# Kernel optimization log

Measured on AMD Instinct MI355X. Metric: run time of the kernel, lower is better.

The kernel has to match this reference:

```python
import jax, jax.numpy as jnp
import numpy as np


def setup_inputs() -> dict:
    key = jax.random.key(0)
    ks = jax.random.split(key, 8)
    B, S, Nc, C, Cseed = 4, 4096, 8192, 512, 256
    return {
        "query_xyz": jax.random.normal(ks[0], (B, S, 3), dtype=jnp.float32),
        "ref_xyz": jax.random.normal(ks[1], (B, Nc, 3), dtype=jnp.float32),
        "ref_feat": jax.random.normal(ks[2], (B, C, Nc), dtype=jnp.float32),
        "seed_features": jax.random.normal(ks[3], (B, Cseed, S), dtype=jnp.float32),
        "W_seed_proj": jax.random.normal(ks[4], (Cseed, C), dtype=jnp.float32) * 0.02,
        "b_seed_proj": jax.random.normal(ks[5], (Cseed,), dtype=jnp.float32) * 0.02,
        "W_concat_proj": jax.random.normal(ks[6], (Cseed, 2 * Cseed), dtype=jnp.float32) * 0.02,
        "b_concat_proj": jax.random.normal(ks[7], (Cseed,), dtype=jnp.float32) * 0.02,
    }


def _nn_gather(query_xyz, ref_xyz, ref_feat):
    # torch.cdist(p=2) + argmin: argmin over squared distance is identical
    # (sqrt is monotonic), so we skip the sqrt.
    q2 = jnp.sum(query_xyz * query_xyz, axis=-1, keepdims=True)      # (B,S,1)
    r2 = jnp.sum(ref_xyz * ref_xyz, axis=-1)[:, None, :]             # (B,1,Nc)
    qr = jnp.einsum("bsd,bnd->bsn", query_xyz, ref_xyz)              # (B,S,Nc)
    d2 = q2 + r2 - 2.0 * qr                                          # (B,S,Nc)
    idx = jnp.argmin(d2, axis=-1)                                    # (B,S) int
    # gather nearest-neighbor features: (B,C,Nc) -> (B,C,S)
    return jnp.take_along_axis(ref_feat, idx[:, None, :], axis=2)


def reference(query_xyz, ref_xyz, ref_feat, seed_features,
              W_seed_proj, b_seed_proj, W_concat_proj, b_concat_proj):
    lift3d_raw = _nn_gather(query_xyz, ref_xyz, ref_feat)            # (B,C,S)
    # 1x1 Conv1d == channel matmul
    lift3d_seed = jnp.einsum("oc,bcs->bos", W_seed_proj, lift3d_raw) \
                  + b_seed_proj[None, :, None]                       # (B,256,S)
    fused = jnp.concatenate([seed_features, lift3d_seed], axis=1)    # (B,512,S)
    out = jnp.einsum("oc,bcs->bos", W_concat_proj, fused) \
          + b_concat_proj[None, :, None]                             # (B,256,S)
    return out
```

## Files before the change

### kernel.cpp

```cpp
#include <hip/hip_runtime.h>

#define B_   4
#define S_   4096
#define NC   8192
#define C_   512
#define CS   256
#define KTOT 768

typedef __attribute__((ext_vector_type(8))) short short8;
typedef __attribute__((ext_vector_type(4))) float f32x4;

static __device__ __forceinline__ unsigned short f2bf(float x) {
    unsigned u = __builtin_bit_cast(unsigned, x);
    unsigned r = u + 0x7FFFu + ((u >> 16) & 1u);
    return (unsigned short)(r >> 16);
}

__global__ __launch_bounds__(256) void prep_kernel(
        const float* __restrict__ rxyz, float4* __restrict__ refpk,
        const float* __restrict__ Wcat, const float* __restrict__ Wseed,
        unsigned short* __restrict__ Wcomb,
        const float* __restrict__ bseed, const float* __restrict__ bcat,
        float* __restrict__ beff) {
    __shared__ float sa[64][68];
    __shared__ float sbt[64][68];
    int bid = blockIdx.x;
    int tid = threadIdx.x;

    if (bid < 64) {
        int w = tid >> 6, l = tid & 63;
        int o = bid * 4 + w;
        float4 wv = *(const float4*)(Wcat + (size_t)o * 512 + 256 + l * 4);
        float4 bb = *(const float4*)(bseed + l * 4);
        float acc = __fmul_rn(wv.x, bb.x);
        acc = fmaf(wv.y, bb.y, acc);
        acc = fmaf(wv.z, bb.z, acc);
        acc = fmaf(wv.w, bb.w, acc);
        #pragma unroll
        for (int off = 32; off > 0; off >>= 1) acc += __shfl_down(acc, off);
        if (l == 0) beff[o] = acc + bcat[o];
    } else if (bid < 96) {
        int xb = bid - 64;
        int tc = (xb & 7) * 64;
        int to = (xb >> 3) * 64;
        int tx = tid & 15, ty = tid >> 4;
        float acc[4][4] = {};
        for (int kt = 0; kt < 256; kt += 64) {
            __syncthreads();
            #pragma unroll
            for (int r = 0; r < 4; ++r) {
                int oo = r * 16 + ty;
                float4 v = *(const float4*)(Wcat + (size_t)(to + oo) * 512 + 256 + kt + tx * 4);
                sa[oo][tx * 4 + 0] = v.x;
                sa[oo][tx * 4 + 1] = v.y;
                sa[oo][tx * 4 + 2] = v.z;
                sa[oo][tx * 4 + 3] = v.w;
                float4 u = *(const float4*)(Wseed + (size_t)(kt + oo) * 512 + tc + tx * 4);
                sbt[oo][tx * 4 + 0] = u.x;
                sbt[oo][tx * 4 + 1] = u.y;
                sbt[oo][tx * 4 + 2] = u.z;
                sbt[oo][tx * 4 + 3] = u.w;
            }
            __syncthreads();
            for (int k = 0; k < 64; ++k) {
                float a[4], bb2[4];
                #pragma unroll
                for (int i = 0; i < 4; ++i) a[i] = sa[ty * 4 + i][k];
                #pragma unroll
                for (int j = 0; j < 4; ++j) bb2[j] = sbt[k][tx * 4 + j];
                #pragma unroll
                for (int i = 0; i < 4; ++i)
                    #pragma unroll
                    for (int j = 0; j < 4; ++j)
                        acc[i][j] = fmaf(a[i], bb2[j], acc[i][j]);
            }
        }
        #pragma unroll
        for (int i = 0; i < 4; ++i)
            #pragma unroll
            for (int j = 0; j < 4; ++j)
                Wcomb[(size_t)(to + ty * 4 + i) * KTOT + 256 + tc + tx * 4 + j] = f2bf(acc[i][j]);
    } else if (bid < 160) {
        int g = ((bid - 96) * 256 + tid) * 4;
        int o = g >> 8, cc = g & 255;
        float4 v = *(const float4*)(Wcat + (size_t)o * 512 + cc);
        ushort4 ov;
        ov.x = f2bf(v.x); ov.y = f2bf(v.y); ov.z = f2bf(v.z); ov.w = f2bf(v.w);
        *(ushort4*)(Wcomb + (size_t)o * KTOT + cc) = ov;
    } else {
        int gid = (bid - 160) * 256 + tid;
        float x = rxyz[gid * 3 + 0];
        float y = rxyz[gid * 3 + 1];
        float z = rxyz[gid * 3 + 2];
        float r2 = __fadd_rn(__fadd_rn(__fmul_rn(x, x), __fmul_rn(y, y)), __fmul_rn(z, z));
        refpk[gid] = make_float4(x, y, z, r2);
    }
}

__global__ __launch_bounds__(256, 4) void mid_kernel(
        const float* __restrict__ qxyz, const float4* __restrict__ refpk,
        float* __restrict__ pval, int* __restrict__ pidx,
        const float* __restrict__ rf, unsigned short* __restrict__ refT) {
    __shared__ float t[64][65];
    int bid = blockIdx.x;
    int tid = threadIdx.x;

    if (bid % 3 != 0) {
        int id = bid - bid / 3 - 1;
        int b = id >> 10;
        int c0 = ((id >> 7) & 7) * 64;
        int n0 = (id & 127) * 64;
        int tx = tid & 15, ty = tid >> 4;
        #pragma unroll
        for (int r = 0; r < 4; ++r) {
            int cc = r * 16 + ty;
            float4 v = *(const float4*)(rf + ((size_t)b * C_ + c0 + cc) * NC + n0 + tx * 4);
            t[tx * 4 + 0][cc] = v.x;
            t[tx * 4 + 1][cc] = v.y;
            t[tx * 4 + 2][cc] = v.z;
            t[tx * 4 + 3][cc] = v.w;
        }
        __syncthreads();
        #pragma unroll
        for (int r = 0; r < 4; ++r) {
            int n = r * 16 + ty;
            ushort4 o;
            o.x = f2bf(t[n][tx * 4 + 0]);
            o.y = f2bf(t[n][tx * 4 + 1]);
            o.z = f2bf(t[n][tx * 4 + 2]);
            o.w = f2bf(t[n][tx * 4 + 3]);
            *(ushort4*)(refT + ((size_t)b * NC + n0 + n) * C_ + c0 + tx * 4) = o;
        }
    } else {
        int aid = bid / 3;
        int sblk = aid & 127;
        int c = (aid >> 7) & 3;
        int b = aid >> 9;
        int lane = tid & 63;
        int qg = tid >> 6;
        int sbase = sblk * 32 + qg * 8;

        float qx[8], qy[8], qz[8], q2[8];
        #pragma unroll
        for (int q = 0; q < 8; ++q) {
            const float* qp = qxyz + ((size_t)(b * S_ + sbase + q)) * 3;
            qx[q] = qp[0]; qy[q] = qp[1]; qz[q] = qp[2];
            q2[q] = __fadd_rn(__fadd_rn(__fmul_rn(qx[q], qx[q]), __fmul_rn(qy[q], qy[q])),
                              __fmul_rn(qz[q], qz[q]));
        }

        const float4* ep = refpk + (size_t)b * NC + c * 2048 + lane;
        float best[8];
        int bj[8];
        #pragma unroll
        for (int q = 0; q < 8; ++q) { best[q] = 3.4028235e38f; bj[q] = 0; }

        float4 r0 = ep[0];
        float4 r1 = ep[64];
        #pragma unroll 2
        for (int j = 0; j < 32; j += 2) {
            float4 r2 = r0, r3 = r1;
            if (j + 2 < 32) {
                r2 = ep[(j + 2) * 64];
                r3 = ep[(j + 3) * 64];
            }
            #pragma unroll
            for (int q = 0; q < 8; ++q) {
                float qr = __fadd_rn(__fadd_rn(__fmul_rn(qx[q], r0.x), __fmul_rn(qy[q], r0.y)),
                                     __fmul_rn(qz[q], r0.z));
                float s = __fadd_rn(q2[q], r0.w);
                float d2 = fmaf(qr, -2.0f, s);
                if (d2 < best[q]) { best[q] = d2; bj[q] = j; }
            }
            #pragma unroll
            for (int q = 0; q < 8; ++q) {
                float qr = __fadd_rn(__fadd_rn(__fmul_rn(qx[q], r1.x), __fmul_rn(qy[q], r1.y)),
                                     __fmul_rn(qz[q], r1.z));
                float s = __fadd_rn(q2[q], r1.w);
                float d2 = fmaf(qr, -2.0f, s);
                if (d2 < best[q]) { best[q] = d2; bj[q] = j + 1; }
            }
            r0 = r2;
            r1 = r3;
        }

        int bx[8];
        #pragma unroll
        for (int q = 0; q < 8; ++q) bx[q] = c * 2048 + bj[q] * 64 + lane;

        #pragma unroll
        for (int m = 1; m < 64; m <<= 1) {
            #pragma unroll
            for (int q = 0; q < 8; ++q) {
                float vv = __shfl_xor(best[q], m, 64);
                int xx = __shfl_xor(bx[q], m, 64);
                if (vv < best[q] || (vv == best[q] && xx < bx[q])) {
                    best[q] = vv; bx[q] = xx;
                }
            }
        }
        if (lane == 0) {
            #pragma unroll
            for (int q = 0; q < 8; ++q) {
                int qs = b * S_ + sbase + q;
                pval[qs * 4 + c] = best[q];
                pidx[qs * 4 + c] = bx[q];
            }
        }
    }
}

__global__ __launch_bounds__(256) void fused_gemm_kernel(
        const unsigned short* __restrict__ Wcomb,
        const float* __restrict__ seed,
        const unsigned short* __restrict__ refT,
        const float* __restrict__ pval,
        const int* __restrict__ pidx,
        const float* __restrict__ beff,
        float* __restrict__ out) {
    __shared__ __align__(16) unsigned short sA[2][128][72];
    __shared__ __align__(16) unsigned short sB[2][32][72];
    __shared__ int sIdx[32];
    __shared__ float sBias[128];

    int tid = threadIdx.x;
    int b = blockIdx.z;
    int m0 = blockIdx.y * 128;
    int s0 = blockIdx.x * 32;
    if (tid < 32) {
        int qs = b * S_ + s0 + tid;
        float v = pval[qs * 4 + 0];
        int x = pidx[qs * 4 + 0];
        #pragma unroll
        for (int c = 1; c < 4; ++c) {
            float vv = pval[qs * 4 + c];
            int xx = pidx[qs * 4 + c];
            if (vv < v || (vv == v && xx < x)) { v = vv; x = xx; }
        }
        sIdx[tid] = x & (NC - 1);
    }
    if (tid < 128) sBias[tid] = beff[m0 + tid];

    int lane = tid & 63;
    int w = tid >> 6;
    int ln = lane & 15;
    int quad = lane >> 4;
    int q8 = quad * 8;

    int mmb  = tid >> 3;
    int kk8a = (tid & 7) << 3;
    const unsigned short* Arow = Wcomb + (size_t)(m0 + mmb) * KTOT + kk8a;
    int n_s  = tid & 31;
    int kk8s = (tid >> 5) << 3;
    int n_g  = tid >> 3;

    f32x4 acc[2][2];
    #pragma unroll
    for (int i = 0; i < 2; ++i)
        #pragma unroll
        for (int j = 0; j < 2; ++j)
            acc[i][j] = (f32x4){0.f, 0.f, 0.f, 0.f};

    short8 ra[4];
    short8 rb;
    float rbf[8];

    #define SLOAD(PK) do {                                                         \
        int pk0 = (PK) * 64;                                                       \
        _Pragma("unroll")                                                          \
        for (int i = 0; i < 4; ++i)                                                \
            ra[i] = *(const short8*)(Arow + (size_t)i * 32 * KTOT + pk0);          \
        if (pk0 < 256) {                                                           \
            const float* sp = seed + ((size_t)b * CS + pk0 + kk8s) * S_ + s0 + n_s;\
            _Pragma("unroll")                                                      \
            for (int r = 0; r < 8; ++r) rbf[r] = sp[(size_t)r * S_];               \
        } else {                                                                   \
            rb = *(const short8*)(refT + ((size_t)b * NC + sIdx[n_g]) * C_         \
                                  + (pk0 - 256) + kk8a);                           \
        }                                                                          \
    } while (0)

    #define SWRITE(BUF, PK) do {                                                   \
        int pk0 = (PK) * 64;                                                       \
        _Pragma("unroll")                                                          \
        for (int i = 0; i < 4; ++i)                                                \
            *(short8*)&sA[BUF][mmb + 32 * i][kk8a] = ra[i];                        \
        if (pk0 < 256) {                                                           \
            unsigned short tmp[8];                                                 \
            _Pragma("unroll")                                                      \
            for (int r = 0; r < 8; ++r) tmp[r] = f2bf(rbf[r]);                     \
            *(short8*)&sB[BUF][n_s][kk8s] = *(const short8*)tmp;                   \
        } else {                                                                   \
            *(short8*)&sB[BUF][n_g][kk8a] = rb;                                    \
        }                                                                          \
    } while (0)

    SLOAD(0);
    SWRITE(0, 0);
    __syncthreads();

    int cur = 0;
    for (int ks = 0; ks < 12; ++ks) {
        if (ks < 11) SLOAD(ks + 1);
        #pragma unroll
        for (int kf = 0; kf < 2; ++kf) {
            short8 af[2], bfr[2];
            #pragma unroll
            for (int i = 0; i < 2; ++i)
                af[i] = *(const short8*)&sA[cur][w * 32 + i * 16 + ln][kf * 32 + q8];
            #pragma unroll
            for (int j = 0; j < 2; ++j)
                bfr[j] = *(const short8*)&sB[cur][j * 16 + ln][kf * 32 + q8];
            #pragma unroll
            for (int i = 0; i < 2; ++i)
                #pragma unroll
                for (int j = 0; j < 2; ++j)
                    acc[i][j] = __builtin_amdgcn_mfma_f32_16x16x32_bf16(af[i], bfr[j], acc[i][j], 0, 0, 0);
        }
        if (ks < 11) {
            SWRITE(cur ^ 1, ks + 1);
            __syncthreads();
            cur ^= 1;
        }
    }
    #undef SLOAD
    #undef SWRITE

    #pragma unroll
    for (int i = 0; i < 2; ++i) {
        int mb = w * 32 + i * 16 + quad * 4;
        #pragma unroll
        for (int j = 0; j < 2; ++j) {
            int col = s0 + j * 16 + ln;
            #pragma unroll
            for (int r = 0; r < 4; ++r) {
                int m = mb + r;
                out[((size_t)b * CS + m0 + m) * S_ + col] = acc[i][j][r] + sBias[m];
            }
        }
    }
}

extern "C" void kernel_launch(void* const* d_in, const int* in_sizes, int n_in,
                              void* d_out, int out_size, void* d_ws, size_t ws_size,
                              hipStream_t stream) {
    const float* qxyz  = (const float*)d_in[0];
    const float* rxyz  = (const float*)d_in[1];
    const float* rfeat = (const float*)d_in[2];
    const float* seed  = (const float*)d_in[3];
    const float* Wseed = (const float*)d_in[4];
    const float* bseed = (const float*)d_in[5];
    const float* Wcat  = (const float*)d_in[6];
    const float* bcat  = (const float*)d_in[7];
    float* out = (float*)d_out;

    char* ws = (char*)d_ws;
    float* pval           = (float*)(ws);
    int* pidx             = (int*)(ws + 262144);
    float* beff           = (float*)(ws + 524288);
    float4* refpk         = (float4*)(ws + 528384);
    unsigned short* Wcomb = (unsigned short*)(ws + 1052672);
    unsigned short* refT  = (unsigned short*)(ws + 1445888);

    hipLaunchKernelGGL(prep_kernel, dim3(288), dim3(256), 0, stream,
                       rxyz, refpk, Wcat, Wseed, Wcomb, bseed, bcat, beff);
    hipLaunchKernelGGL(mid_kernel, dim3(6144), dim3(256), 0, stream,
                       qxyz, refpk, pval, pidx, rfeat, refT);
    hipLaunchKernelGGL(fused_gemm_kernel, dim3(128, 2, 4), dim3(256), 0, stream,
                       Wcomb, seed, refT, pval, pidx, beff, out);
}
```

Before: 189.2 us.

## Move seed-feature GEMM half into mid kernel, overlapping with NN search

The seed_features half of the concat projection (K=256) moves out of the final GEMM. A new prep stage transposes seed into bf16 seedT, and mid_kernel gains a third block type that computes the Wcomb[:, :256] x seedT partial product and writes it to out, running alongside the NN search and refT transpose blocks. The final GEMM then only covers the gathered refT half (8 k-steps instead of 12) and adds the partial result read back from out. This trades an extra read and write of out, plus a seed transpose pass, for a shorter critical-path GEMM and for overlapping independent work. It also drops the occupancy hint on mid_kernel.

```diff
diff --git a/kernel.cpp b/kernel.cpp
--- a/kernel.cpp
+++ b/kernel.cpp
@@ -21,7 +21,8 @@
         const float* __restrict__ Wcat, const float* __restrict__ Wseed,
         unsigned short* __restrict__ Wcomb,
         const float* __restrict__ bseed, const float* __restrict__ bcat,
-        float* __restrict__ beff) {
+        float* __restrict__ beff,
+        const float* __restrict__ seed, unsigned short* __restrict__ seedT) {
     __shared__ float sa[64][68];
     __shared__ float sbt[64][68];
     int bid = blockIdx.x;
@@ -87,26 +88,179 @@
         ushort4 ov;
         ov.x = f2bf(v.x); ov.y = f2bf(v.y); ov.z = f2bf(v.z); ov.w = f2bf(v.w);
         *(ushort4*)(Wcomb + (size_t)o * KTOT + cc) = ov;
-    } else {
+    } else if (bid < 288) {
         int gid = (bid - 160) * 256 + tid;
         float x = rxyz[gid * 3 + 0];
         float y = rxyz[gid * 3 + 1];
         float z = rxyz[gid * 3 + 2];
         float r2 = __fadd_rn(__fadd_rn(__fmul_rn(x, x), __fmul_rn(y, y)), __fmul_rn(z, z));
         refpk[gid] = make_float4(x, y, z, r2);
+    } else {
+        int id = bid - 288;
+        int b = id >> 8;
+        int rem = id & 255;
+        int c0 = (rem >> 6) * 64;
+        int s0 = (rem & 63) * 64;
+        int tx = tid & 15, ty = tid >> 4;
+        #pragma unroll
+        for (int r = 0; r < 4; ++r) {
+            int cc = r * 16 + ty;
+            float4 v = *(const float4*)(seed + ((size_t)b * CS + c0 + cc) * S_ + s0 + tx * 4);
+            sa[tx * 4 + 0][cc] = v.x;
+            sa[tx * 4 + 1][cc] = v.y;
+            sa[tx * 4 + 2][cc] = v.z;
+            sa[tx * 4 + 3][cc] = v.w;
+        }
+        __syncthreads();
+        #pragma unroll
+        for (int r = 0; r < 4; ++r) {
+            int n = r * 16 + ty;
+            ushort4 o;
+            o.x = f2bf(sa[n][tx * 4 + 0]);
+            o.y = f2bf(sa[n][tx * 4 + 1]);
+            o.z = f2bf(sa[n][tx * 4 + 2]);
+            o.w = f2bf(sa[n][tx * 4 + 3]);
+            *(ushort4*)(seedT + ((size_t)b * S_ + s0 + n) * CS + c0 + tx * 4) = o;
+        }
     }
 }
 
-__global__ __launch_bounds__(256, 4) void mid_kernel(
+__global__ __launch_bounds__(256) void mid_kernel(
         const float* __restrict__ qxyz, const float4* __restrict__ refpk,
         float* __restrict__ pval, int* __restrict__ pidx,
-        const float* __restrict__ rf, unsigned short* __restrict__ refT) {
-    __shared__ float t[64][65];
+        const float* __restrict__ rf, unsigned short* __restrict__ refT,
+        const unsigned short* __restrict__ Wcomb,
+        const unsigned short* __restrict__ seedT,
+        float* __restrict__ out) {
+    __shared__ __align__(16) char smem[16640];
     int bid = blockIdx.x;
     int tid = threadIdx.x;
-
-    if (bid % 3 != 0) {
-        int id = bid - bid / 3 - 1;
+    int r4 = bid & 3;
+    int g = bid >> 2;
+
+    if (r4 == 0) {
+        int aid = g;
+        int sblk = aid & 127;
+        int c = (aid >> 7) & 3;
+        int b = aid >> 9;
+        int lane = tid & 63;
+        int qg = tid >> 6;
+        int sbase = sblk * 32 + qg * 8;
+
+        float qx[8], qy[8], qz[8], q2[8];
+        #pragma unroll
+        for (int q = 0; q < 8; ++q) {
+            const float* qp = qxyz + ((size_t)(b * S_ + sbase + q)) * 3;
+            qx[q] = qp[0]; qy[q] = qp[1]; qz[q] = qp[2];
+            q2[q] = __fadd_rn(__fadd_rn(__fmul_rn(qx[q], qx[q]), __fmul_rn(qy[q], qy[q])),
+                              __fmul_rn(qz[q], qz[q]));
+        }
+
+        const float4* ep = refpk + (size_t)b * NC + c * 2048 + lane;
+        float best[8];
+        int bj[8];
+        #pragma unroll
+        for (int q = 0; q < 8; ++q) { best[q] = 3.4028235e38f; bj[q] = 0; }
+
+        float4 r0 = ep[0];
+        float4 r1 = ep[64];
+        #pragma unroll 2
+        for (int j = 0; j < 32; j += 2) {
+            float4 r2 = r0, r3 = r1;
+            if (j + 2 < 32) {
+                r2 = ep[(j + 2) * 64];
+                r3 = ep[(j + 3) * 64];
+            }
+            #pragma unroll
+            for (int q = 0; q < 8; ++q) {
+                float qr = __fadd_rn(__fadd_rn(__fmul_rn(qx[q], r0.x), __fmul_rn(qy[q], r0.y)),
+                                     __fmul_rn(qz[q], r0.z));
+                float s = __fadd_rn(q2[q], r0.w);
+                float d2 = fmaf(qr, -2.0f, s);
+                if (d2 < best[q]) { best[q] = d2; bj[q] = j; }
+            }
+            #pragma unroll
+            for (int q = 0; q < 8; ++q) {
+                float qr = __fadd_rn(__fadd_rn(__fmul_rn(qx[q], r1.x), __fmul_rn(qy[q], r1.y)),
+                                     __fmul_rn(qz[q], r1.z));
+                float s = __fadd_rn(q2[q], r1.w);
+                float d2 = fmaf(qr, -2.0f, s);
+                if (d2 < best[q]) { best[q] = d2; bj[q] = j + 1; }
+            }
+            r0 = r2;
+            r1 = r3;
+        }
+
+        int bx[8];
+        #pragma unroll
+        for (int q = 0; q < 8; ++q) bx[q] = c * 2048 + bj[q] * 64 + lane;
+
+        #pragma unroll
+        for (int m = 1; m < 64; m <<= 1) {
+            #pragma unroll
+            for (int q = 0; q < 8; ++q) {
+                float vv = __shfl_xor(best[q], m, 64);
+                int xx = __shfl_xor(bx[q], m, 64);
+                if (vv < best[q] || (vv == best[q] && xx < bx[q])) {
+                    best[q] = vv; bx[q] = xx;
+                }
+            }
+        }
+        if (lane == 0) {
+            #pragma unroll
+            for (int q = 0; q < 8; ++q) {
+                int qs = b * S_ + sbase + q;
+                pval[qs * 4 + c] = best[q];
+                pidx[qs * 4 + c] = bx[q];
+            }
+        }
+    } else if (r4 == 2) {
+        unsigned short (*sAw)[72] = (unsigned short (*)[72])smem;
+        unsigned short (*sBw)[72] = (unsigned short (*)[72])(smem + 9216);
+        int b = g >> 9;
+        int rem = g & 511;
+        int m0 = (rem >> 7) * 64;
+        int s0 = (rem & 127) * 32;
+        int lane = tid & 63;
+        int w = tid >> 6;
+        int ln = lane & 15;
+        int quad = lane >> 4;
+        int q8 = quad * 8;
+        int mm = tid >> 2, kk16 = (tid & 3) << 4;
+        int n = tid >> 3, kk8 = (tid & 7) << 3;
+        const unsigned short* Ar = Wcomb + (size_t)(m0 + mm) * KTOT + kk16;
+        const unsigned short* Br = seedT + ((size_t)b * S_ + s0 + n) * CS + kk8;
+
+        f32x4 acc2[2];
+        acc2[0] = (f32x4){0.f, 0.f, 0.f, 0.f};
+        acc2[1] = (f32x4){0.f, 0.f, 0.f, 0.f};
+        for (int kt = 0; kt < 4; ++kt) {
+            __syncthreads();
+            *(short8*)&sAw[mm][kk16]     = *(const short8*)(Ar + kt * 64);
+            *(short8*)&sAw[mm][kk16 + 8] = *(const short8*)(Ar + kt * 64 + 8);
+            *(short8*)&sBw[n][kk8]       = *(const short8*)(Br + kt * 64);
+            __syncthreads();
+            #pragma unroll
+            for (int kf = 0; kf < 2; ++kf) {
+                short8 af = *(const short8*)&sAw[w * 16 + ln][kf * 32 + q8];
+                #pragma unroll
+                for (int j = 0; j < 2; ++j) {
+                    short8 bfr = *(const short8*)&sBw[j * 16 + ln][kf * 32 + q8];
+                    acc2[j] = __builtin_amdgcn_mfma_f32_16x16x32_bf16(af, bfr, acc2[j], 0, 0, 0);
+                }
+            }
+        }
+        int mb = m0 + w * 16 + quad * 4;
+        #pragma unroll
+        for (int j = 0; j < 2; ++j) {
+            int col = s0 + j * 16 + ln;
+            #pragma unroll
+            for (int r = 0; r < 4; ++r)
+                out[((size_t)b * CS + mb + r) * S_ + col] = acc2[j][r];
+        }
+    } else {
+        float (*t)[65] = (float (*)[65])smem;
+        int id = g * 2 + (r4 >> 1);
         int b = id >> 10;
         int c0 = ((id >> 7) & 7) * 64;
         int n0 = (id & 127) * 64;
@@ -131,88 +285,11 @@
             o.w = f2bf(t[n][tx * 4 + 3]);
             *(ushort4*)(refT + ((size_t)b * NC + n0 + n) * C_ + c0 + tx * 4) = o;
         }
-    } else {
-        int aid = bid / 3;
-        int sblk = aid & 127;
-        int c = (aid >> 7) & 3;
-        int b = aid >> 9;
-        int lane = tid & 63;
-        int qg = tid >> 6;
-        int sbase = sblk * 32 + qg * 8;
-
-        float qx[8], qy[8], qz[8], q2[8];
-        #pragma unroll
-        for (int q = 0; q < 8; ++q) {
-            const float* qp = qxyz + ((size_t)(b * S_ + sbase + q)) * 3;
-            qx[q] = qp[0]; qy[q] = qp[1]; qz[q] = qp[2];
-            q2[q] = __fadd_rn(__fadd_rn(__fmul_rn(qx[q], qx[q]), __fmul_rn(qy[q], qy[q])),
-                              __fmul_rn(qz[q], qz[q]));
-        }
-
-        const float4* ep = refpk + (size_t)b * NC + c * 2048 + lane;
-        float best[8];
-        int bj[8];
-        #pragma unroll
-        for (int q = 0; q < 8; ++q) { best[q] = 3.4028235e38f; bj[q] = 0; }
-
-        float4 r0 = ep[0];
-        float4 r1 = ep[64];
-        #pragma unroll 2
-        for (int j = 0; j < 32; j += 2) {
-            float4 r2 = r0, r3 = r1;
-            if (j + 2 < 32) {
-                r2 = ep[(j + 2) * 64];
-                r3 = ep[(j + 3) * 64];
-            }
-            #pragma unroll
-            for (int q = 0; q < 8; ++q) {
-                float qr = __fadd_rn(__fadd_rn(__fmul_rn(qx[q], r0.x), __fmul_rn(qy[q], r0.y)),
-                                     __fmul_rn(qz[q], r0.z));
-                float s = __fadd_rn(q2[q], r0.w);
-                float d2 = fmaf(qr, -2.0f, s);
-                if (d2 < best[q]) { best[q] = d2; bj[q] = j; }
-            }
-            #pragma unroll
-            for (int q = 0; q < 8; ++q) {
-                float qr = __fadd_rn(__fadd_rn(__fmul_rn(qx[q], r1.x), __fmul_rn(qy[q], r1.y)),
-                                     __fmul_rn(qz[q], r1.z));
-                float s = __fadd_rn(q2[q], r1.w);
-                float d2 = fmaf(qr, -2.0f, s);
-                if (d2 < best[q]) { best[q] = d2; bj[q] = j + 1; }
-            }
-            r0 = r2;
-            r1 = r3;
-        }
-
-        int bx[8];
-        #pragma unroll
-        for (int q = 0; q < 8; ++q) bx[q] = c * 2048 + bj[q] * 64 + lane;
-
-        #pragma unroll
-        for (int m = 1; m < 64; m <<= 1) {
-            #pragma unroll
-            for (int q = 0; q < 8; ++q) {
-                float vv = __shfl_xor(best[q], m, 64);
-                int xx = __shfl_xor(bx[q], m, 64);
-                if (vv < best[q] || (vv == best[q] && xx < bx[q])) {
-                    best[q] = vv; bx[q] = xx;
-                }
-            }
-        }
-        if (lane == 0) {
-            #pragma unroll
-            for (int q = 0; q < 8; ++q) {
-                int qs = b * S_ + sbase + q;
-                pval[qs * 4 + c] = best[q];
-                pidx[qs * 4 + c] = bx[q];
-            }
-        }
     }
 }
 
 __global__ __launch_bounds__(256) void fused_gemm_kernel(
         const unsigned short* __restrict__ Wcomb,
-        const float* __restrict__ seed,
         const unsigned short* __restrict__ refT,
         const float* __restrict__ pval,
         const int* __restrict__ pidx,
@@ -249,9 +326,7 @@
 
     int mmb  = tid >> 3;
     int kk8a = (tid & 7) << 3;
-    const unsigned short* Arow = Wcomb + (size_t)(m0 + mmb) * KTOT + kk8a;
-    int n_s  = tid & 31;
-    int kk8s = (tid >> 5) << 3;
+    const unsigned short* Arow = Wcomb + (size_t)(m0 + mmb) * KTOT + 256 + kk8a;
     int n_g  = tid >> 3;
 
     f32x4 acc[2][2];
@@ -263,45 +338,31 @@
 
     short8 ra[4];
     short8 rb;
-    float rbf[8];
 
     #define SLOAD(PK) do {                                                         \
         int pk0 = (PK) * 64;                                                       \
         _Pragma("unroll")                                                          \
         for (int i = 0; i < 4; ++i)                                                \
             ra[i] = *(const short8*)(Arow + (size_t)i * 32 * KTOT + pk0);          \
-        if (pk0 < 256) {                                                           \
-            const float* sp = seed + ((size_t)b * CS + pk0 + kk8s) * S_ + s0 + n_s;\
-            _Pragma("unroll")                                                      \
-            for (int r = 0; r < 8; ++r) rbf[r] = sp[(size_t)r * S_];               \
-        } else {                                                                   \
-            rb = *(const short8*)(refT + ((size_t)b * NC + sIdx[n_g]) * C_         \
-                                  + (pk0 - 256) + kk8a);                           \
-        }                                                                          \
+        rb = *(const short8*)(refT + ((size_t)b * NC + sIdx[n_g]) * C_             \
+                              + pk0 + kk8a);                                       \
     } while (0)
 
-    #define SWRITE(BUF, PK) do {                                                   \
-        int pk0 = (PK) * 64;                                                       \
+    #define SWRITE(BUF) do {                                                       \
         _Pragma("unroll")                                                          \
         for (int i = 0; i < 4; ++i)                                                \
             *(short8*)&sA[BUF][mmb + 32 * i][kk8a] = ra[i];                        \
-        if (pk0 < 256) {                                                           \
-            unsigned short tmp[8];                                                 \
-            _Pragma("unroll")                                                      \
-            for (int r = 0; r < 8; ++r) tmp[r] = f2bf(rbf[r]);                     \
-            *(short8*)&sB[BUF][n_s][kk8s] = *(const short8*)tmp;                   \
-        } else {                                                                   \
-            *(short8*)&sB[BUF][n_g][kk8a] = rb;                                    \
-        }                                                                          \
+        *(short8*)&sB[BUF][n_g][kk8a] = rb;                                        \
     } while (0)
 
+    __syncthreads();
     SLOAD(0);
-    SWRITE(0, 0);
+    SWRITE(0);
     __syncthreads();
 
     int cur = 0;
-    for (int ks = 0; ks < 12; ++ks) {
-        if (ks < 11) SLOAD(ks + 1);
+    for (int ks = 0; ks < 8; ++ks) {
+        if (ks < 7) SLOAD(ks + 1);
         #pragma unroll
         for (int kf = 0; kf < 2; ++kf) {
             short8 af[2], bfr[2];
@@ -317,8 +378,8 @@
                 for (int j = 0; j < 2; ++j)
                     acc[i][j] = __builtin_amdgcn_mfma_f32_16x16x32_bf16(af[i], bfr[j], acc[i][j], 0, 0, 0);
         }
-        if (ks < 11) {
-            SWRITE(cur ^ 1, ks + 1);
+        if (ks < 7) {
+            SWRITE(cur ^ 1);
             __syncthreads();
             cur ^= 1;
         }
@@ -335,7 +396,8 @@
             #pragma unroll
             for (int r = 0; r < 4; ++r) {
                 int m = mb + r;
-                out[((size_t)b * CS + m0 + m) * S_ + col] = acc[i][j][r] + sBias[m];
+                size_t oaddr = ((size_t)b * CS + m0 + m) * S_ + col;
+                out[oaddr] = acc[i][j][r] + sBias[m] + out[oaddr];
             }
         }
     }
@@ -361,11 +423,12 @@
     float4* refpk         = (float4*)(ws + 528384);
     unsigned short* Wcomb = (unsigned short*)(ws + 1052672);
     unsigned short* refT  = (unsigned short*)(ws + 1445888);
-
-    hipLaunchKernelGGL(prep_kernel, dim3(288), dim3(256), 0, stream,
-                       rxyz, refpk, Wcat, Wseed, Wcomb, bseed, bcat, beff);
-    hipLaunchKernelGGL(mid_kernel, dim3(6144), dim3(256), 0, stream,
-                       qxyz, refpk, pval, pidx, rfeat, refT);
+    unsigned short* seedT = (unsigned short*)(ws + 35000320);
+
+    hipLaunchKernelGGL(prep_kernel, dim3(1312), dim3(256), 0, stream,
+                       rxyz, refpk, Wcat, Wseed, Wcomb, bseed, bcat, beff, seed, seedT);
+    hipLaunchKernelGGL(mid_kernel, dim3(8192), dim3(256), 0, stream,
+                       qxyz, refpk, pval, pidx, rfeat, refT, Wcomb, seedT, out);
     hipLaunchKernelGGL(fused_gemm_kernel, dim3(128, 2, 4), dim3(256), 0, stream,
-                       Wcomb, seed, refT, pval, pidx, beff, out);
+                       Wcomb, refT, pval, pidx, beff, out);
 }
```

New measurement: 251.9 us. 1.33x slower.

## Pre-transpose seed features to bf16 and retile fused GEMM to 64x64 single-buffered

Applied to the files above, without the earlier changes.

Adds blocks to the prep kernel that transpose seed_features into an S-major bf16 buffer. The fused GEMM can then load both B sources with contiguous 16-byte vector loads instead of strided fp32 reads converted in-kernel. The GEMM tile changes from 128x32 to 64x64 with a 2x2 wave layout, and the double-buffered register prefetch is removed in favour of a simple sync-load-sync loop. The cost is an extra transpose pass over seed data and less overlap between global loads and MFMA work.

```diff
diff --git a/kernel.cpp b/kernel.cpp
--- a/kernel.cpp
+++ b/kernel.cpp
@@ -21,7 +21,8 @@
         const float* __restrict__ Wcat, const float* __restrict__ Wseed,
         unsigned short* __restrict__ Wcomb,
         const float* __restrict__ bseed, const float* __restrict__ bcat,
-        float* __restrict__ beff) {
+        float* __restrict__ beff,
+        const float* __restrict__ seed, unsigned short* __restrict__ seedT) {
     __shared__ float sa[64][68];
     __shared__ float sbt[64][68];
     int bid = blockIdx.x;
@@ -87,13 +88,40 @@
         ushort4 ov;
         ov.x = f2bf(v.x); ov.y = f2bf(v.y); ov.z = f2bf(v.z); ov.w = f2bf(v.w);
         *(ushort4*)(Wcomb + (size_t)o * KTOT + cc) = ov;
-    } else {
+    } else if (bid < 288) {
         int gid = (bid - 160) * 256 + tid;
         float x = rxyz[gid * 3 + 0];
         float y = rxyz[gid * 3 + 1];
         float z = rxyz[gid * 3 + 2];
         float r2 = __fadd_rn(__fadd_rn(__fmul_rn(x, x), __fmul_rn(y, y)), __fmul_rn(z, z));
         refpk[gid] = make_float4(x, y, z, r2);
+    } else {
+        int id = bid - 288;
+        int b = id >> 8;
+        int rem = id & 255;
+        int c0 = (rem >> 6) * 64;
+        int s0 = (rem & 63) * 64;
+        int tx = tid & 15, ty = tid >> 4;
+        #pragma unroll
+        for (int r = 0; r < 4; ++r) {
+            int cc = r * 16 + ty;
+            float4 v = *(const float4*)(seed + ((size_t)b * CS + c0 + cc) * S_ + s0 + tx * 4);
+            sa[tx * 4 + 0][cc] = v.x;
+            sa[tx * 4 + 1][cc] = v.y;
+            sa[tx * 4 + 2][cc] = v.z;
+            sa[tx * 4 + 3][cc] = v.w;
+        }
+        __syncthreads();
+        #pragma unroll
+        for (int r = 0; r < 4; ++r) {
+            int n = r * 16 + ty;
+            ushort4 o;
+            o.x = f2bf(sa[n][tx * 4 + 0]);
+            o.y = f2bf(sa[n][tx * 4 + 1]);
+            o.z = f2bf(sa[n][tx * 4 + 2]);
+            o.w = f2bf(sa[n][tx * 4 + 3]);
+            *(ushort4*)(seedT + ((size_t)b * S_ + s0 + n) * CS + c0 + tx * 4) = o;
+        }
     }
 }
 
@@ -212,22 +240,22 @@
 
 __global__ __launch_bounds__(256) void fused_gemm_kernel(
         const unsigned short* __restrict__ Wcomb,
-        const float* __restrict__ seed,
+        const unsigned short* __restrict__ seedT,
         const unsigned short* __restrict__ refT,
         const float* __restrict__ pval,
         const int* __restrict__ pidx,
         const float* __restrict__ beff,
         float* __restrict__ out) {
-    __shared__ __align__(16) unsigned short sA[2][128][72];
-    __shared__ __align__(16) unsigned short sB[2][32][72];
-    __shared__ int sIdx[32];
-    __shared__ float sBias[128];
+    __shared__ __align__(16) unsigned short sA[64][72];
+    __shared__ __align__(16) unsigned short sB[64][72];
+    __shared__ int sIdx[64];
+    __shared__ float sBias[64];
 
     int tid = threadIdx.x;
     int b = blockIdx.z;
-    int m0 = blockIdx.y * 128;
-    int s0 = blockIdx.x * 32;
-    if (tid < 32) {
+    int m0 = blockIdx.y * 64;
+    int s0 = blockIdx.x * 64;
+    if (tid < 64) {
         int qs = b * S_ + s0 + tid;
         float v = pval[qs * 4 + 0];
         int x = pidx[qs * 4 + 0];
@@ -238,21 +266,21 @@
             if (vv < v || (vv == v && xx < x)) { v = vv; x = xx; }
         }
         sIdx[tid] = x & (NC - 1);
-    }
-    if (tid < 128) sBias[tid] = beff[m0 + tid];
+        sBias[tid] = beff[m0 + tid];
+    }
 
     int lane = tid & 63;
     int w = tid >> 6;
+    int wm = w >> 1;
+    int wn = w & 1;
     int ln = lane & 15;
     int quad = lane >> 4;
     int q8 = quad * 8;
 
-    int mmb  = tid >> 3;
-    int kk8a = (tid & 7) << 3;
-    const unsigned short* Arow = Wcomb + (size_t)(m0 + mmb) * KTOT + kk8a;
-    int n_s  = tid & 31;
-    int kk8s = (tid >> 5) << 3;
-    int n_g  = tid >> 3;
+    int mm   = tid >> 2;
+    int kk16 = (tid & 3) << 4;
+    const unsigned short* Arow = Wcomb + (size_t)(m0 + mm) * KTOT + kk16;
+    const unsigned short* Srow = seedT + ((size_t)b * S_ + s0 + mm) * CS + kk16;
 
     f32x4 acc[2][2];
     #pragma unroll
@@ -261,77 +289,40 @@
         for (int j = 0; j < 2; ++j)
             acc[i][j] = (f32x4){0.f, 0.f, 0.f, 0.f};
 
-    short8 ra[4];
-    short8 rb;
-    float rbf[8];
-
-    #define SLOAD(PK) do {                                                         \
-        int pk0 = (PK) * 64;                                                       \
-        _Pragma("unroll")                                                          \
-        for (int i = 0; i < 4; ++i)                                                \
-            ra[i] = *(const short8*)(Arow + (size_t)i * 32 * KTOT + pk0);          \
-        if (pk0 < 256) {                                                           \
-            const float* sp = seed + ((size_t)b * CS + pk0 + kk8s) * S_ + s0 + n_s;\
-            _Pragma("unroll")                                                      \
-            for (int r = 0; r < 8; ++r) rbf[r] = sp[(size_t)r * S_];               \
-        } else {                                                                   \
-            rb = *(const short8*)(refT + ((size_t)b * NC + sIdx[n_g]) * C_         \
-                                  + (pk0 - 256) + kk8a);                           \
-        }                                                                          \
-    } while (0)
-
-    #define SWRITE(BUF, PK) do {                                                   \
-        int pk0 = (PK) * 64;                                                       \
-        _Pragma("unroll")                                                          \
-        for (int i = 0; i < 4; ++i)                                                \
-            *(short8*)&sA[BUF][mmb + 32 * i][kk8a] = ra[i];                        \
-        if (pk0 < 256) {                                                           \
-            unsigned short tmp[8];                                                 \
-            _Pragma("unroll")                                                      \
-            for (int r = 0; r < 8; ++r) tmp[r] = f2bf(rbf[r]);                     \
-            *(short8*)&sB[BUF][n_s][kk8s] = *(const short8*)tmp;                   \
-        } else {                                                                   \
-            *(short8*)&sB[BUF][n_g][kk8a] = rb;                                    \
-        }                                                                          \
-    } while (0)
-
-    SLOAD(0);
-    SWRITE(0, 0);
-    __syncthreads();
-
-    int cur = 0;
     for (int ks = 0; ks < 12; ++ks) {
-        if (ks < 11) SLOAD(ks + 1);
+        int k0 = ks * 64;
+        __syncthreads();
+        *(short8*)&sA[mm][kk16]     = *(const short8*)(Arow + k0);
+        *(short8*)&sA[mm][kk16 + 8] = *(const short8*)(Arow + k0 + 8);
+        const unsigned short* Brow =
+            (k0 < 256) ? (Srow + k0)
+                       : (refT + ((size_t)b * NC + sIdx[mm]) * C_ + (k0 - 256) + kk16);
+        *(short8*)&sB[mm][kk16]     = *(const short8*)(Brow);
+        *(short8*)&sB[mm][kk16 + 8] = *(const short8*)(Brow + 8);
+        __syncthreads();
         #pragma unroll
         for (int kf = 0; kf < 2; ++kf) {
             short8 af[2], bfr[2];
             #pragma unroll
             for (int i = 0; i < 2; ++i)
-                af[i] = *(const short8*)&sA[cur][w * 32 + i * 16 + ln][kf * 32 + q8];
+                af[i] = *(const short8*)&sA[wm * 32 + i * 16 + ln][kf * 32 + q8];
             #pragma unroll
             for (int j = 0; j < 2; ++j)
-                bfr[j] = *(const short8*)&sB[cur][j * 16 + ln][kf * 32 + q8];
+                bfr[j] = *(const short8*)&sB[wn * 32 + j * 16 + ln][kf * 32 + q8];
             #pragma unroll
             for (int i = 0; i < 2; ++i)
                 #pragma unroll
                 for (int j = 0; j < 2; ++j)
                     acc[i][j] = __builtin_amdgcn_mfma_f32_16x16x32_bf16(af[i], bfr[j], acc[i][j], 0, 0, 0);
         }
-        if (ks < 11) {
-            SWRITE(cur ^ 1, ks + 1);
-            __syncthreads();
-            cur ^= 1;
-        }
-    }
-    #undef SLOAD
-    #undef SWRITE
+    }
 
     #pragma unroll
     for (int i = 0; i < 2; ++i) {
-        int mb = w * 32 + i * 16 + quad * 4;
+        int mb = wm * 32 + i * 16 + quad * 4;
         #pragma unroll
         for (int j = 0; j < 2; ++j) {
-            int col = s0 + j * 16 + ln;
+            int col = s0 + wn * 32 + j * 16 + ln;
             #pragma unroll
             for (int r = 0; r < 4; ++r) {
                 int m = mb + r;
@@ -361,11 +352,12 @@
     float4* refpk         = (float4*)(ws + 528384);
     unsigned short* Wcomb = (unsigned short*)(ws + 1052672);
     unsigned short* refT  = (unsigned short*)(ws + 1445888);
-
-    hipLaunchKernelGGL(prep_kernel, dim3(288), dim3(256), 0, stream,
-                       rxyz, refpk, Wcat, Wseed, Wcomb, bseed, bcat, beff);
+    unsigned short* seedT = (unsigned short*)(ws + 35000320);
+
+    hipLaunchKernelGGL(prep_kernel, dim3(1312), dim3(256), 0, stream,
+                       rxyz, refpk, Wcat, Wseed, Wcomb, bseed, bcat, beff, seed, seedT);
     hipLaunchKernelGGL(mid_kernel, dim3(6144), dim3(256), 0, stream,
                        qxyz, refpk, pval, pidx, rfeat, refT);
-    hipLaunchKernelGGL(fused_gemm_kernel, dim3(128, 2, 4), dim3(256), 0, stream,
-                       Wcomb, seed, refT, pval, pidx, beff, out);
-}
+    hipLaunchKernelGGL(fused_gemm_kernel, dim3(64, 4, 4), dim3(256), 0, stream,
+                       Wcomb, seedT, refT, pval, pidx, beff, out);
+}
```

New measurement: 183.3 us. -3.1%, faster.
